# Performance work log

Measured on AMD Instinct MI355X. Metric: run time of the kernel, lower is better.

The kernel has to match this reference:

```python
import jax, jax.numpy as jnp
import numpy as np

D_MODEL = 1024
HEADS = 16
HEAD_DIM = D_MODEL // HEADS
FF = 4 * D_MODEL
EPS = 1e-5


def _layer_norm(x, g, b):
    mu = jnp.mean(x, axis=-1, keepdims=True)
    var = jnp.mean(jnp.square(x - mu), axis=-1, keepdims=True)
    return (x - mu) * jax.lax.rsqrt(var + EPS) * g + b


def setup_inputs() -> dict:
    key = jax.random.key(0)
    ks = jax.random.split(key, 12)
    s = 0.02
    inp = {
        "x": jax.random.normal(ks[0], (2, 2048, D_MODEL), dtype=jnp.float32),
        "Wq": jax.random.normal(ks[1], (D_MODEL, D_MODEL), dtype=jnp.float32) * s,
        "bq": jnp.zeros((D_MODEL,), jnp.float32),
        "Wk": jax.random.normal(ks[2], (D_MODEL, D_MODEL), dtype=jnp.float32) * s,
        "bk": jnp.zeros((D_MODEL,), jnp.float32),
        "Wv": jax.random.normal(ks[3], (D_MODEL, D_MODEL), dtype=jnp.float32) * s,
        "bv": jnp.zeros((D_MODEL,), jnp.float32),
        "Wm": jax.random.normal(ks[4], (D_MODEL, D_MODEL), dtype=jnp.float32) * s,
        "bm": jnp.zeros((D_MODEL,), jnp.float32),
        "W1": jax.random.normal(ks[5], (D_MODEL, FF), dtype=jnp.float32) * s,
        "b1": jnp.zeros((FF,), jnp.float32),
        "W2": jax.random.normal(ks[6], (FF, D_MODEL), dtype=jnp.float32) * s,
        "b2": jnp.zeros((D_MODEL,), jnp.float32),
        "g1": jnp.ones((D_MODEL,), jnp.float32),
        "be1": jnp.zeros((D_MODEL,), jnp.float32),
        "g2": jnp.ones((D_MODEL,), jnp.float32),
        "be2": jnp.zeros((D_MODEL,), jnp.float32),
    }
    return inp


def reference(x, Wq, bq, Wk, bk, Wv, bv, Wm, bm, W1, b1, W2, b2, g1, be1, g2, be2):
    B, L, _ = x.shape
    # self-attention: source = x, no pos, no masks
    q = (x @ Wq + bq).reshape(B, L, HEADS, HEAD_DIM).transpose(0, 2, 1, 3)
    k = (x @ Wk + bk).reshape(B, L, HEADS, HEAD_DIM).transpose(0, 2, 1, 3)
    v = (x @ Wv + bv).reshape(B, L, HEADS, HEAD_DIM).transpose(0, 2, 1, 3)
    scale = 1.0 / np.sqrt(HEAD_DIM).astype(np.float32)
    scores = jnp.einsum("bhld,bhsd->bhls", q, k) * scale  # [B,H,L,L]
    attn = jax.nn.softmax(scores, axis=-1)
    msg = jnp.einsum("bhls,bhsd->bhld", attn, v)
    msg = msg.transpose(0, 2, 1, 3).reshape(B, L, D_MODEL)
    msg = msg @ Wm + bm
    h = _layer_norm(x + msg, g1, be1)
    ffn = jax.nn.relu(h @ W1 + b1) @ W2 + b2
    return _layer_norm(h + ffn, g2, be2)
```

## Files before the change

### kernel.cpp

```cpp
#include <hip/hip_runtime.h>

#define D_MODEL 1024
#define N_TOK   4096
#define HEADS   16
#define FF_DIM  4096
#define SEQ_L   2048

typedef unsigned short u16;
typedef unsigned int   u32;
typedef __bf16 bf16x8 __attribute__((ext_vector_type(8)));
typedef float  f32x4  __attribute__((ext_vector_type(4)));

#define AS1C(p) ((const __attribute__((address_space(1))) void*)(p))
#define AS3(p)  ((__attribute__((address_space(3))) void*)(p))

__device__ __forceinline__ u16 f2bf(float f) {
    union { float f; unsigned u; } c; c.f = f;
    return (u16)((c.u + 0x7fffu + ((c.u >> 16) & 1u)) >> 16);
}
__device__ __forceinline__ float bf2f(u16 b) {
    union { unsigned u; float f; } c; c.u = ((unsigned)b) << 16;
    return c.f;
}
__device__ __forceinline__ u32 cvt_pk_bf16(float lo, float hi) {
    u32 r;
    asm("v_cvt_pk_bf16_f32 %0, %1, %2" : "=v"(r) : "v"(lo), "v"(hi));
    return r;
}
__device__ __forceinline__ float fmax3(float a, float b, float c) {
    float r;
    asm("v_max3_f32 %0, %1, %2, %3" : "=v"(r) : "v"(a), "v"(b), "v"(c));
    return r;
}

template<int RELU>
__global__ __launch_bounds__(512, 2)
void gemm_pipe(const u16* __restrict__ A, const u16* __restrict__ Bt,
               const float* __restrict__ bias, u16* __restrict__ C,
               int M, int N, int K)
{
    __shared__ u16 As[2][256 * 64];
    __shared__ u16 Bs[2][256 * 64];

    const int tid = threadIdx.x;
    const int wid = tid >> 6, lane = tid & 63;
    const int wr  = wid >> 2, wc = wid & 3;
    const int l15 = lane & 15, l16 = lane >> 4;

    const int nwg = gridDim.x * gridDim.y;
    int bid = blockIdx.y * gridDim.x + blockIdx.x;
    bid = (bid & 7) * (nwg >> 3) + (bid >> 3);
    const int r0 = (bid / gridDim.x) * 256, c0 = (bid % gridDim.x) * 256;

    const u16* Ab = A  + (size_t)r0 * K;
    const u16* Bb = Bt + (size_t)c0 * K;

    f32x4 acc[8][4];
#pragma unroll
    for (int m = 0; m < 8; ++m)
#pragma unroll
        for (int n = 0; n < 4; ++n) acc[m][n] = (f32x4){0.f, 0.f, 0.f, 0.f};

    auto stage = [&](u16* dst, const u16* src, int kbase) {
#pragma unroll
        for (int i = 0; i < 4; ++i) {
            const int r  = i * 64 + (tid >> 3);
            const int gc = (tid & 7) ^ (r & 7);
            __builtin_amdgcn_global_load_lds(AS1C(src + (size_t)r * K + kbase + gc * 8),
                                             AS3(dst + (i * 64 + (wid << 3)) * 64), 16, 0, 0);
        }
    };

    bf16x8 af[4][2], bbA[2][2], bbB[2][2];

    auto ldAf = [&](const u16* sl, int mh) {
#pragma unroll
        for (int m = 0; m < 4; ++m) {
            const int row = wr * 128 + (mh * 4 + m) * 16 + l15;
#pragma unroll
            for (int ks = 0; ks < 2; ++ks) {
                const int ch = (ks * 4 + l16) ^ (row & 7);
                af[m][ks] = *(const bf16x8*)&sl[row * 64 + ch * 8];
            }
        }
    };
    auto ldBf = [&](const u16* sl, int pair, bf16x8 (&bb)[2][2]) {
#pragma unroll
        for (int n = 0; n < 2; ++n) {
            const int row = wc * 64 + (pair * 2 + n) * 16 + l15;
#pragma unroll
            for (int ks = 0; ks < 2; ++ks) {
                const int ch = (ks * 4 + l16) ^ (row & 7);
                bb[n][ks] = *(const bf16x8*)&sl[row * 64 + ch * 8];
            }
        }
    };
    auto mm16 = [&](int mh, int pair, bf16x8 (&bb)[2][2]) {
        __builtin_amdgcn_s_setprio(1);
#pragma unroll
        for (int ks = 0; ks < 2; ++ks)
#pragma unroll
            for (int m = 0; m < 4; ++m)
#pragma unroll
                for (int n = 0; n < 2; ++n)
                    acc[mh * 4 + m][pair * 2 + n] =
                        __builtin_amdgcn_mfma_f32_16x16x32_bf16(af[m][ks], bb[n][ks],
                                                                acc[mh * 4 + m][pair * 2 + n], 0, 0, 0);
        __builtin_amdgcn_s_setprio(0);
    };

    const int nt = K >> 6;
    stage(&As[0][0], Ab, 0);
    stage(&Bs[0][0], Bb, 0);
    stage(&As[1][0], Ab, 64);

    for (int t = 0; t < nt; ++t) {
        u16* Asl = &As[t & 1][0];
        u16* Bsl = &Bs[t & 1][0];
        u16* Aso = &As[t & 1][0];
        u16* Bso = &Bs[(t + 1) & 1][0];

        if (t + 1 < nt) { asm volatile("s_waitcnt vmcnt(4)" ::: "memory"); }
        else            { asm volatile("s_waitcnt vmcnt(0)" ::: "memory"); }
        __builtin_amdgcn_s_barrier();
        ldAf(Asl, 0);
        ldBf(Bsl, 0, bbA);
        if (t + 1 < nt) stage(Bso, Bb, (t + 1) * 64);
        __builtin_amdgcn_s_barrier();
        mm16(0, 0, bbA);
        __builtin_amdgcn_s_barrier();
        ldBf(Bsl, 1, bbB);
        mm16(0, 1, bbB);
        __builtin_amdgcn_s_barrier();
        ldAf(Asl, 1);
        mm16(1, 0, bbA);
        __builtin_amdgcn_s_barrier();
        if (t + 2 < nt) stage(Aso, Ab, (t + 2) * 64);
        mm16(1, 1, bbB);
        __builtin_amdgcn_s_barrier();
    }

#pragma unroll
    for (int n = 0; n < 4; ++n) {
        const int col = c0 + wc * 64 + n * 16 + l15;
        const float bv = bias[col];
#pragma unroll
        for (int m = 0; m < 8; ++m) {
#pragma unroll
            for (int r = 0; r < 4; ++r) {
                const size_t row = (size_t)(r0 + wr * 128 + m * 16 + l16 * 4 + r);
                float v = acc[m][n][r] + bv;
                if (RELU) v = fmaxf(v, 0.f);
                C[row * N + col] = f2bf(v);
            }
        }
    }
}

template<int RELU>
__global__ __launch_bounds__(512, 2)
void gemm_pipe128(const u16* __restrict__ A, const u16* __restrict__ Bt,
                  const float* __restrict__ bias, u16* __restrict__ C,
                  int M, int N, int K)
{
    __shared__ u16 As[2][128 * 64];
    __shared__ u16 Bs[2][128 * 64];

    const int tid = threadIdx.x;
    const int wid = tid >> 6, lane = tid & 63;
    const int wr  = wid >> 2, wc = wid & 3;
    const int l15 = lane & 15, l16 = lane >> 4;

    const int nwg = gridDim.x * gridDim.y;
    int bid = blockIdx.y * gridDim.x + blockIdx.x;
    bid = (bid & 7) * (nwg >> 3) + (bid >> 3);
    const int r0 = (bid / gridDim.x) * 128, c0 = (bid % gridDim.x) * 128;

    const u16* Ab = A  + (size_t)r0 * K;
    const u16* Bb = Bt + (size_t)c0 * K;

    f32x4 acc[4][2];
#pragma unroll
    for (int m = 0; m < 4; ++m)
#pragma unroll
        for (int n = 0; n < 2; ++n) acc[m][n] = (f32x4){0.f, 0.f, 0.f, 0.f};

    auto stage = [&](u16* dst, const u16* src, int kbase) {
#pragma unroll
        for (int i = 0; i < 2; ++i) {
            const int r  = i * 64 + (tid >> 3);
            const int gc = (tid & 7) ^ (r & 7);
            __builtin_amdgcn_global_load_lds(AS1C(src + (size_t)r * K + kbase + gc * 8),
                                             AS3(dst + (i * 64 + (wid << 3)) * 64), 16, 0, 0);
        }
    };

    const int nt = K >> 6;
    stage(&As[0][0], Ab, 0);  stage(&Bs[0][0], Bb, 0);
    stage(&As[1][0], Ab, 64); stage(&Bs[1][0], Bb, 64);

    for (int t = 0; t < nt; ++t) {
        const u16* Asl = &As[t & 1][0];
        const u16* Bsl = &Bs[t & 1][0];

        if (t + 1 < nt) { asm volatile("s_waitcnt vmcnt(4)" ::: "memory"); }
        else            { asm volatile("s_waitcnt vmcnt(0)" ::: "memory"); }
        __builtin_amdgcn_s_barrier();

        bf16x8 af[4][2], bb[2][2];
#pragma unroll
        for (int m = 0; m < 4; ++m) {
            const int row = wr * 64 + m * 16 + l15;
#pragma unroll
            for (int ks = 0; ks < 2; ++ks) {
                const int ch = (ks * 4 + l16) ^ (row & 7);
                af[m][ks] = *(const bf16x8*)&Asl[row * 64 + ch * 8];
            }
        }
#pragma unroll
        for (int n = 0; n < 2; ++n) {
            const int row = wc * 32 + n * 16 + l15;
#pragma unroll
            for (int ks = 0; ks < 2; ++ks) {
                const int ch = (ks * 4 + l16) ^ (row & 7);
                bb[n][ks] = *(const bf16x8*)&Bsl[row * 64 + ch * 8];
            }
        }
        __builtin_amdgcn_s_setprio(1);
#pragma unroll
        for (int ks = 0; ks < 2; ++ks)
#pragma unroll
            for (int m = 0; m < 4; ++m)
#pragma unroll
                for (int n = 0; n < 2; ++n)
                    acc[m][n] = __builtin_amdgcn_mfma_f32_16x16x32_bf16(af[m][ks], bb[n][ks], acc[m][n], 0, 0, 0);
        __builtin_amdgcn_s_setprio(0);
        __builtin_amdgcn_s_barrier();

        if (t + 2 < nt) {
            stage(&As[t & 1][0], Ab, (t + 2) * 64);
            stage(&Bs[t & 1][0], Bb, (t + 2) * 64);
        }
    }

#pragma unroll
    for (int n = 0; n < 2; ++n) {
        const int col = c0 + wc * 32 + n * 16 + l15;
        const float bv = bias[col];
#pragma unroll
        for (int m = 0; m < 4; ++m) {
#pragma unroll
            for (int r = 0; r < 4; ++r) {
                const size_t row = (size_t)(r0 + wr * 64 + m * 16 + l16 * 4 + r);
                float v = acc[m][n][r] + bv;
                if (RELU) v = fmaxf(v, 0.f);
                C[row * N + col] = f2bf(v);
            }
        }
    }
}

__global__ __launch_bounds__(512, 4)
void attn_mfma(const u16* __restrict__ qkv, u16* __restrict__ ao)
{
    __shared__ u16 Kl[64 * 64];
    __shared__ u32 Vt[64 * 32];

    const int tid = threadIdx.x;
    const int wid = tid >> 6, lane = tid & 63;
    const int l15 = lane & 15, l16 = lane >> 4;
    const int bh  = blockIdx.y, b = bh >> 4, h = bh & 15;
    const int ho  = h * 64;
    const size_t tb = (size_t)b * SEQ_L;
    const int q0  = blockIdx.x * 128;

    const u16* qg = qkv + (tb + q0) * 3072 + ho;
    const u16* kg = qkv + tb * 3072 + 1024 + ho;
    const u16* vg = qkv + tb * 3072 + 2048 + ho;

    const float SC = 0.18033688f;

    bf16x8 qa[2];
#pragma unroll
    for (int ks = 0; ks < 2; ++ks) {
        union { bf16x8 v; u16 u[8]; u32 w[4]; } a, r;
        a.v = *(const bf16x8*)(qg + (size_t)(wid * 16 + l15) * 3072 + ks * 32 + l16 * 8);
#pragma unroll
        for (int e = 0; e < 4; ++e)
            r.w[e] = cvt_pk_bf16(bf2f(a.u[2 * e]) * SC, bf2f(a.u[2 * e + 1]) * SC);
        qa[ks] = r.v;
    }

    const int sp = tid & 31;
    const int dc = tid >> 5;

    f32x4 oacc[4];
#pragma unroll
    for (int f = 0; f < 4; ++f) oacc[f] = (f32x4){0.f, 0.f, 0.f, 0.f};
    float m_c = -1e30f, l_c = 0.f;

    for (int s0 = 0; s0 < SEQ_L; s0 += 64) {
        ushort4 ua4 = *(const ushort4*)(vg + (size_t)(s0 + 2 * sp) * 3072 + dc * 4);
        ushort4 ub4 = *(const ushort4*)(vg + (size_t)(s0 + 2 * sp + 1) * 3072 + dc * 4);

        __syncthreads();
        {
            const int r  = tid >> 3;
            const int gc = (tid & 7) ^ (r & 7);
            __builtin_amdgcn_global_load_lds(AS1C(kg + (size_t)(s0 + r) * 3072 + gc * 8),
                                             AS3(&Kl[(wid * 8) * 64]), 16, 0, 0);
        }
        {
            const u16* pu = (const u16*)&ua4;
            const u16* pv = (const u16*)&ub4;
#pragma unroll
            for (int e = 0; e < 4; ++e) {
                const int d = dc * 4 + e;
                const int w = sp ^ (((d & 7) << 2) ^ ((d >> 3) << 1));
                Vt[d * 32 + w] = (u32)pu[e] | ((u32)pv[e] << 16);
            }
        }
        __syncthreads();

        f32x4 sacc[4];
#pragma unroll
        for (int f = 0; f < 4; ++f) sacc[f] = (f32x4){0.f, 0.f, 0.f, 0.f};
#pragma unroll
        for (int ks = 0; ks < 2; ++ks)
#pragma unroll
            for (int f = 0; f < 4; ++f) {
                const int row = f * 16 + l15;
                const int ch  = (ks * 4 + l16) ^ (row & 7);
                bf16x8 kb = *(const bf16x8*)&Kl[row * 64 + ch * 8];
                sacc[f] = __builtin_amdgcn_mfma_f32_16x16x32_bf16(kb, qa[ks], sacc[f], 0, 0, 0);
            }

        float mx;
        {
            float a0 = fmax3(sacc[0][0], sacc[0][1], sacc[0][2]);
            float a1 = fmax3(sacc[0][3], sacc[1][0], sacc[1][1]);
            float a2 = fmax3(sacc[1][2], sacc[1][3], sacc[2][0]);
            float a3 = fmax3(sacc[2][1], sacc[2][2], sacc[2][3]);
            float a4 = fmax3(sacc[3][0], sacc[3][1], sacc[3][2]);
            float b0 = fmax3(a0, a1, sacc[3][3]);
            float b1 = fmax3(a2, a3, a4);
            mx = fmaxf(b0, b1);
        }
        mx = fmaxf(mx, __shfl_xor(mx, 16));
        mx = fmaxf(mx, __shfl_xor(mx, 32));

        if (__any(mx > m_c + 8.f)) {
            const float mnew = fmaxf(m_c, mx);
            const float corr = __builtin_exp2f(m_c - mnew);
            m_c = mnew;
            l_c *= corr;
#pragma unroll
            for (int r = 0; r < 4; ++r) {
                const float cr = __shfl(corr, l16 * 4 + r);
#pragma unroll
                for (int f = 0; f < 4; ++f) oacc[f][r] *= cr;
            }
        }

        float rs = 0.f;
#pragma unroll
        for (int f = 0; f < 4; ++f)
#pragma unroll
            for (int r = 0; r < 4; ++r) {
                const float p = __builtin_exp2f(sacc[f][r] - m_c);
                sacc[f][r] = p; rs += p;
            }
        rs += __shfl_xor(rs, 16);
        rs += __shfl_xor(rs, 32);
        l_c += rs;

        u32 pk[4][2];
#pragma unroll
        for (int f = 0; f < 4; ++f) {
            pk[f][0] = cvt_pk_bf16(sacc[f][0], sacc[f][1]);
            pk[f][1] = cvt_pk_bf16(sacc[f][2], sacc[f][3]);
        }

#pragma unroll
        for (int S = 0; S < 2; ++S) {
            union { bf16x8 v; u32 u[4]; } af;
            af.u[0] = pk[2 * S][0];     af.u[1] = pk[2 * S][1];
            af.u[2] = pk[2 * S + 1][0]; af.u[3] = pk[2 * S + 1][1];
#pragma unroll
            for (int f2 = 0; f2 < 4; ++f2) {
                const int d = f2 * 16 + l15;
                const int swzd = ((d & 7) << 2) ^ ((d >> 3) << 1);
                union { bf16x8 v; uint2 u[2]; } vb;
                vb.u[0] = *(const uint2*)&Vt[d * 32 + ((16 * S + 2 * l16) ^ swzd)];
                vb.u[1] = *(const uint2*)&Vt[d * 32 + ((16 * S + 8 + 2 * l16) ^ swzd)];
                oacc[f2] = __builtin_amdgcn_mfma_f32_16x16x32_bf16(af.v, vb.v, oacc[f2], 0, 0, 0);
            }
        }
    }

#pragma unroll
    for (int r = 0; r < 4; ++r) {
        const float ld  = __shfl(l_c, l16 * 4 + r);
        const float inv = 1.f / ld;
        const size_t row = tb + q0 + wid * 16 + l16 * 4 + r;
#pragma unroll
        for (int f2 = 0; f2 < 4; ++f2)
            ao[row * 1024 + ho + f2 * 16 + l15] = f2bf(oacc[f2][r] * inv);
    }
}

template<int WB>
__global__ __launch_bounds__(256)
void add_ln(const float* __restrict__ x, const u16* __restrict__ y,
            const float* __restrict__ g, const float* __restrict__ be,
            float* __restrict__ outf, u16* __restrict__ outb)
{
    __shared__ float red[4];
    const int t = blockIdx.x, tid = threadIdx.x;
    const int c = tid * 4, lane = tid & 63, wv = tid >> 6;

    float4 a = *(const float4*)(x + (size_t)t * D_MODEL + c);
    ushort4 yb = *(const ushort4*)(y + (size_t)t * D_MODEL + c);
    float s[4] = {a.x + bf2f(yb.x), a.y + bf2f(yb.y), a.z + bf2f(yb.z), a.w + bf2f(yb.w)};

    float ps = s[0] + s[1] + s[2] + s[3];
#pragma unroll
    for (int off = 32; off > 0; off >>= 1) ps += __shfl_down(ps, off);
    if (lane == 0) red[wv] = ps;
    __syncthreads();
    const float mean = (red[0] + red[1] + red[2] + red[3]) * (1.f / D_MODEL);
    __syncthreads();

    float pv = 0.f;
#pragma unroll
    for (int u = 0; u < 4; ++u) { float d = s[u] - mean; pv += d * d; }
#pragma unroll
    for (int off = 32; off > 0; off >>= 1) pv += __shfl_down(pv, off);
    if (lane == 0) red[wv] = pv;
    __syncthreads();
    const float var = (red[0] + red[1] + red[2] + red[3]) * (1.f / D_MODEL);
    const float inv = rsqrtf(var + 1e-5f);

    float4 g4 = *(const float4*)(g + c);
    float4 b4 = *(const float4*)(be + c);
    float o[4];
#pragma unroll
    for (int u = 0; u < 4; ++u) o[u] = (s[u] - mean) * inv;
    float4 of = {o[0] * g4.x + b4.x, o[1] * g4.y + b4.y, o[2] * g4.z + b4.z, o[3] * g4.w + b4.w};
    *(float4*)(outf + (size_t)t * D_MODEL + c) = of;
    if (WB) {
        ushort4 ob = {f2bf(of.x), f2bf(of.y), f2bf(of.z), f2bf(of.w)};
        *(ushort4*)(outb + (size_t)t * D_MODEL + c) = ob;
    }
}

__global__ __launch_bounds__(256)
void prep(const float* __restrict__ Wq, const float* __restrict__ Wk,
          const float* __restrict__ Wv, const float* __restrict__ Wm,
          const float* __restrict__ W1, const float* __restrict__ W2,
          const float* __restrict__ x,
          const float* __restrict__ bq, const float* __restrict__ bk,
          const float* __restrict__ bv,
          u16* __restrict__ wqkv_t, u16* __restrict__ wm_t,
          u16* __restrict__ w1_t, u16* __restrict__ w2_t,
          u16* __restrict__ xb, float* __restrict__ bqkv)
{
    const int blk = blockIdx.x, tid = threadIdx.x;
    if (blk < 3072) {
        __shared__ float T[64][65];
        const float* src; u16* dst; int K, N, tile;
        if (blk < 256)       { src = Wq; dst = wqkv_t;               K = 1024; N = 1024; tile = blk; }
        else if (blk < 512)  { src = Wk; dst = wqkv_t + 1024 * 1024; K = 1024; N = 1024; tile = blk - 256; }
        else if (blk < 768)  { src = Wv; dst = wqkv_t + 2*1024*1024; K = 1024; N = 1024; tile = blk - 512; }
        else if (blk < 1024) { src = Wm; dst = wm_t;                 K = 1024; N = 1024; tile = blk - 768; }
        else if (blk < 2048) { src = W1; dst = w1_t;                 K = 1024; N = 4096; tile = blk - 1024; }
        else                 { src = W2; dst = w2_t;                 K = 4096; N = 1024; tile = blk - 2048; }
        const int ntn = N >> 6;
        const int n0 = (tile % ntn) * 64, k0 = (tile / ntn) * 64;
        const int rr = tid >> 4, cc = (tid & 15) * 4;
#pragma unroll
        for (int u = 0; u < 4; ++u) {
            const float4 v = *(const float4*)(src + (size_t)(k0 + rr + u * 16) * N + n0 + cc);
            T[rr + u * 16][cc + 0] = v.x; T[rr + u * 16][cc + 1] = v.y;
            T[rr + u * 16][cc + 2] = v.z; T[rr + u * 16][cc + 3] = v.w;
        }
        __syncthreads();
#pragma unroll
        for (int u = 0; u < 4; ++u) {
            const int n = rr + u * 16;
            ushort4 o;
            o.x = f2bf(T[cc + 0][n]); o.y = f2bf(T[cc + 1][n]);
            o.z = f2bf(T[cc + 2][n]); o.w = f2bf(T[cc + 3][n]);
            *(ushort4*)(dst + (size_t)(n0 + n) * K + k0 + cc) = o;
        }
    } else if (blk < 3072 + 4096) {
        const int i = (blk - 3072) * 1024 + tid * 4;
        float4 v = *(const float4*)(x + i);
        ushort4 o = {f2bf(v.x), f2bf(v.y), f2bf(v.z), f2bf(v.w)};
        *(ushort4*)(xb + i) = o;
    } else {
#pragma unroll
        for (int u = 0; u < 12; ++u) {
            const int i = u * 256 + tid;
            bqkv[i] = i < 1024 ? bq[i] : (i < 2048 ? bk[i - 1024] : bv[i - 2048]);
        }
    }
}

extern "C" void kernel_launch(void* const* d_in, const int* in_sizes, int n_in,
                              void* d_out, int out_size, void* d_ws, size_t ws_size,
                              hipStream_t stream)
{
    (void)in_sizes; (void)n_in; (void)out_size; (void)ws_size;

    const float* x   = (const float*)d_in[0];
    const float* Wq  = (const float*)d_in[1];
    const float* bq  = (const float*)d_in[2];
    const float* Wk  = (const float*)d_in[3];
    const float* bk  = (const float*)d_in[4];
    const float* Wv  = (const float*)d_in[5];
    const float* bv  = (const float*)d_in[6];
    const float* Wm  = (const float*)d_in[7];
    const float* bm  = (const float*)d_in[8];
    const float* W1  = (const float*)d_in[9];
    const float* b1  = (const float*)d_in[10];
    const float* W2  = (const float*)d_in[11];
    const float* b2  = (const float*)d_in[12];
    const float* g1  = (const float*)d_in[13];
    const float* be1 = (const float*)d_in[14];
    const float* g2  = (const float*)d_in[15];
    const float* be2 = (const float*)d_in[16];
    float* out = (float*)d_out;

    char* base = (char*)d_ws;
    const size_t MB = 1u << 20;
    u16*   wqkv_t = (u16*)(base);
    u16*   wm_t   = (u16*)(base + 6 * MB);
    u16*   w1_t   = (u16*)(base + 8 * MB);
    u16*   w2_t   = (u16*)(base + 16 * MB);
    float* bqkv   = (float*)(base + 24 * MB);
    u16*   xb     = (u16*)(base + 25 * MB);
    u16*   qkv    = (u16*)(base + 33 * MB);
    u16*   ao     = (u16*)(base + 57 * MB);
    u16*   f1     = (u16*)(base + 33 * MB);
    u16*   msg    = (u16*)(base + 25 * MB);
    u16*   ffn    = (u16*)(base + 25 * MB);
    float* hf     = (float*)(base + 65 * MB);
    u16*   hb     = (u16*)(base + 81 * MB);

    dim3 blk(256);
    prep<<<dim3(3072 + 4096 + 1), blk, 0, stream>>>(Wq, Wk, Wv, Wm, W1, W2, x,
                                                    bq, bk, bv,
                                                    wqkv_t, wm_t, w1_t, w2_t, xb, bqkv);

    gemm_pipe<0><<<dim3(12, 16), dim3(512), 0, stream>>>(xb, wqkv_t, bqkv, qkv, N_TOK, 3072, 1024);
    attn_mfma<<<dim3(SEQ_L / 128, 32), dim3(512), 0, stream>>>(qkv, ao);
    gemm_pipe128<0><<<dim3(8, 32), dim3(512), 0, stream>>>(ao, wm_t, bm, msg, N_TOK, 1024, 1024);
    add_ln<1><<<dim3(N_TOK), blk, 0, stream>>>(x, msg, g1, be1, hf, hb);
    gemm_pipe<1><<<dim3(16, 16), dim3(512), 0, stream>>>(hb, w1_t, b1, f1, N_TOK, FF_DIM, 1024);
    gemm_pipe128<0><<<dim3(8, 32), dim3(512), 0, stream>>>(f1, w2_t, b2, ffn, N_TOK, 1024, FF_DIM);
    add_ln<0><<<dim3(N_TOK), blk, 0, stream>>>(hf, ffn, g2, be2, out, nullptr);
}
```

Measured before the change: 258.0 us.

## Double-buffer K tiles, widen KV step to 128, and remap attention block order

The attention kernel now processes 128 keys per iteration instead of 64. K is double-buffered in LDS and the next K/V tile is prefetched while the current tile's MFMAs run, so global loads overlap with compute. The block index is also remapped so consecutive blocks spread across heads and batches, which changes L2 locality. LDS use and register pressure go up (sacc doubles to 8 fragments), which may lower occupancy under the 512x4 launch bounds.

```diff
diff --git a/kernel.cpp b/kernel.cpp
--- a/kernel.cpp
+++ b/kernel.cpp
@@ -263,16 +263,19 @@
 __global__ __launch_bounds__(512, 4)
 void attn_mfma(const u16* __restrict__ qkv, u16* __restrict__ ao)
 {
-    __shared__ u16 Kl[64 * 64];
-    __shared__ u32 Vt[64 * 32];
+    __shared__ u16 Kl[2][128 * 64];
+    __shared__ u32 Vt[64 * 64];
 
     const int tid = threadIdx.x;
     const int wid = tid >> 6, lane = tid & 63;
     const int l15 = lane & 15, l16 = lane >> 4;
-    const int bh  = blockIdx.y, b = bh >> 4, h = bh & 15;
-    const int ho  = h * 64;
+
+    int lin = blockIdx.y * gridDim.x + blockIdx.x;
+    lin = (lin & 7) * 64 + (lin >> 3);
+    const int bh = lin >> 4, b = bh >> 4, h = bh & 15;
+    const int q0 = (lin & 15) * 128;
+    const int ho = h * 64;
     const size_t tb = (size_t)b * SEQ_L;
-    const int q0  = blockIdx.x * 128;
 
     const u16* qg = qkv + (tb + q0) * 3072 + ho;
     const u16* kg = qkv + tb * 3072 + 1024 + ho;
@@ -291,60 +294,71 @@
         qa[ks] = r.v;
     }
 
-    const int sp = tid & 31;
-    const int dc = tid >> 5;
+    const int sp = lane;
+    const int dc = wid;
+
+    auto stageK = [&](int buf, int s0) {
+#pragma unroll
+        for (int i = 0; i < 2; ++i) {
+            const int r  = i * 64 + (tid >> 3);
+            const int gc = (tid & 7) ^ (r & 7);
+            __builtin_amdgcn_global_load_lds(AS1C(kg + (size_t)(s0 + r) * 3072 + gc * 8),
+                                             AS3(&Kl[buf][(i * 64 + wid * 8) * 64]), 16, 0, 0);
+        }
+    };
 
     f32x4 oacc[4];
 #pragma unroll
     for (int f = 0; f < 4; ++f) oacc[f] = (f32x4){0.f, 0.f, 0.f, 0.f};
     float m_c = -1e30f, l_c = 0.f;
 
-    for (int s0 = 0; s0 < SEQ_L; s0 += 64) {
-        ushort4 ua4 = *(const ushort4*)(vg + (size_t)(s0 + 2 * sp) * 3072 + dc * 4);
-        ushort4 ub4 = *(const ushort4*)(vg + (size_t)(s0 + 2 * sp + 1) * 3072 + dc * 4);
-
+    union { bf16x8 v; u16 u[8]; } ua, ub;
+    stageK(0, 0);
+    ua.v = *(const bf16x8*)(vg + (size_t)(2 * sp) * 3072 + dc * 8);
+    ub.v = *(const bf16x8*)(vg + (size_t)(2 * sp + 1) * 3072 + dc * 8);
+
+    const int nt = SEQ_L / 128;
+    for (int t = 0; t < nt; ++t) {
+        const int buf = t & 1;
+
+        asm volatile("s_waitcnt vmcnt(0)" ::: "memory");
+#pragma unroll
+        for (int e = 0; e < 8; ++e) {
+            const int d = dc * 8 + e;
+            const int w = sp ^ (((d & 7) << 2) ^ ((d >> 3) << 1));
+            Vt[d * 64 + w] = (u32)ua.u[e] | ((u32)ub.u[e] << 16);
+        }
         __syncthreads();
-        {
-            const int r  = tid >> 3;
-            const int gc = (tid & 7) ^ (r & 7);
-            __builtin_amdgcn_global_load_lds(AS1C(kg + (size_t)(s0 + r) * 3072 + gc * 8),
-                                             AS3(&Kl[(wid * 8) * 64]), 16, 0, 0);
-        }
-        {
-            const u16* pu = (const u16*)&ua4;
-            const u16* pv = (const u16*)&ub4;
-#pragma unroll
-            for (int e = 0; e < 4; ++e) {
-                const int d = dc * 4 + e;
-                const int w = sp ^ (((d & 7) << 2) ^ ((d >> 3) << 1));
-                Vt[d * 32 + w] = (u32)pu[e] | ((u32)pv[e] << 16);
-            }
-        }
-        __syncthreads();
-
-        f32x4 sacc[4];
-#pragma unroll
-        for (int f = 0; f < 4; ++f) sacc[f] = (f32x4){0.f, 0.f, 0.f, 0.f};
+
+        if (t + 1 < nt) {
+            stageK(buf ^ 1, (t + 1) * 128);
+            ua.v = *(const bf16x8*)(vg + (size_t)((t + 1) * 128 + 2 * sp) * 3072 + dc * 8);
+            ub.v = *(const bf16x8*)(vg + (size_t)((t + 1) * 128 + 2 * sp + 1) * 3072 + dc * 8);
+        }
+
+        f32x4 sacc[8];
+#pragma unroll
+        for (int f = 0; f < 8; ++f) sacc[f] = (f32x4){0.f, 0.f, 0.f, 0.f};
 #pragma unroll
         for (int ks = 0; ks < 2; ++ks)
 #pragma unroll
-            for (int f = 0; f < 4; ++f) {
+            for (int f = 0; f < 8; ++f) {
                 const int row = f * 16 + l15;
                 const int ch  = (ks * 4 + l16) ^ (row & 7);
-                bf16x8 kb = *(const bf16x8*)&Kl[row * 64 + ch * 8];
+                bf16x8 kb = *(const bf16x8*)&Kl[buf][row * 64 + ch * 8];
                 sacc[f] = __builtin_amdgcn_mfma_f32_16x16x32_bf16(kb, qa[ks], sacc[f], 0, 0, 0);
             }
 
+        float pm[8];
+#pragma unroll
+        for (int f = 0; f < 8; ++f)
+            pm[f] = fmaxf(fmax3(sacc[f][0], sacc[f][1], sacc[f][2]), sacc[f][3]);
         float mx;
         {
-            float a0 = fmax3(sacc[0][0], sacc[0][1], sacc[0][2]);
-            float a1 = fmax3(sacc[0][3], sacc[1][0], sacc[1][1]);
-            float a2 = fmax3(sacc[1][2], sacc[1][3], sacc[2][0]);
-            float a3 = fmax3(sacc[2][1], sacc[2][2], sacc[2][3]);
-            float a4 = fmax3(sacc[3][0], sacc[3][1], sacc[3][2]);
-            float b0 = fmax3(a0, a1, sacc[3][3]);
-            float b1 = fmax3(a2, a3, a4);
-            mx = fmaxf(b0, b1);
+            float t0 = fmax3(pm[0], pm[1], pm[2]);
+            float t1 = fmax3(pm[3], pm[4], pm[5]);
+            float t2 = fmaxf(pm[6], pm[7]);
+            mx = fmax3(t0, t1, t2);
         }
         mx = fmaxf(mx, __shfl_xor(mx, 16));
         mx = fmaxf(mx, __shfl_xor(mx, 32));
@@ -364,7 +378,7 @@
 
         float rs = 0.f;
 #pragma unroll
-        for (int f = 0; f < 4; ++f)
+        for (int f = 0; f < 8; ++f)
 #pragma unroll
             for (int r = 0; r < 4; ++r) {
                 const float p = __builtin_exp2f(sacc[f][r] - m_c);
@@ -374,15 +388,15 @@
         rs += __shfl_xor(rs, 32);
         l_c += rs;
 
-        u32 pk[4][2];
-#pragma unroll
-        for (int f = 0; f < 4; ++f) {
+        u32 pk[8][2];
+#pragma unroll
+        for (int f = 0; f < 8; ++f) {
             pk[f][0] = cvt_pk_bf16(sacc[f][0], sacc[f][1]);
             pk[f][1] = cvt_pk_bf16(sacc[f][2], sacc[f][3]);
         }
 
 #pragma unroll
-        for (int S = 0; S < 2; ++S) {
+        for (int S = 0; S < 4; ++S) {
             union { bf16x8 v; u32 u[4]; } af;
             af.u[0] = pk[2 * S][0];     af.u[1] = pk[2 * S][1];
             af.u[2] = pk[2 * S + 1][0]; af.u[3] = pk[2 * S + 1][1];
@@ -391,11 +405,12 @@
                 const int d = f2 * 16 + l15;
                 const int swzd = ((d & 7) << 2) ^ ((d >> 3) << 1);
                 union { bf16x8 v; uint2 u[2]; } vb;
-                vb.u[0] = *(const uint2*)&Vt[d * 32 + ((16 * S + 2 * l16) ^ swzd)];
-                vb.u[1] = *(const uint2*)&Vt[d * 32 + ((16 * S + 8 + 2 * l16) ^ swzd)];
+                vb.u[0] = *(const uint2*)&Vt[d * 64 + ((16 * S + 2 * l16) ^ swzd)];
+                vb.u[1] = *(const uint2*)&Vt[d * 64 + ((16 * S + 8 + 2 * l16) ^ swzd)];
                 oacc[f2] = __builtin_amdgcn_mfma_f32_16x16x32_bf16(af.v, vb.v, oacc[f2], 0, 0, 0);
             }
         }
+        __syncthreads();
     }
 
 #pragma unroll
```

Result: no change. 256.2 us (-0.7%).
